# Performance work log

Measured on AMD Instinct MI355X. Metric: run time of the kernel, lower is better.

Reference implementation:

```python
import jax, jax.numpy as jnp
import numpy as np

N, E, G = 40000, 640000, 64
DIN, DH, H, DE = 64, 64, 2, 16
HD = H * DH  # 128
NEG_SLOPE_GAT = 0.2
NEG_SLOPE_ACT = 0.01
EPS_BN = 1e-5


def _p(k, shape, fan_in):
    return jax.random.normal(k, shape, dtype=jnp.float32) * (1.0 / np.sqrt(fan_in))


def setup_inputs() -> dict:
    key = jax.random.key(0)
    ks = jax.random.split(key, 32)
    inp = {
        'x': jax.random.normal(ks[0], (N, DIN), dtype=jnp.float32),
        'edge_index': jax.random.randint(ks[1], (2, E), 0, N, dtype=jnp.int32),
        'edge_attr': jax.random.normal(ks[2], (E, DE), dtype=jnp.float32),
        'batch': jnp.sort(jax.random.randint(ks[3], (N,), 0, G, dtype=jnp.int32)),
    }
    dims_in = [DIN, HD, HD]
    k = 4
    for i in (1, 2, 3):
        din = dims_in[i - 1]
        inp[f'w{i}l'] = _p(ks[k], (din, HD), din); k += 1
        inp[f'w{i}r'] = _p(ks[k], (din, HD), din); k += 1
        inp[f'w{i}e'] = _p(ks[k], (DE, HD), DE); k += 1
        inp[f'a{i}'] = _p(ks[k], (H, DH), DH); k += 1
        inp[f'cb{i}'] = jnp.zeros((HD,), dtype=jnp.float32)
        inp[f'g{i}'] = jnp.ones((HD,), dtype=jnp.float32)
        inp[f'bb{i}'] = jnp.zeros((HD,), dtype=jnp.float32)
    inp['fc1w'] = _p(ks[k], (HD, DH), HD); k += 1
    inp['fc1b'] = jnp.zeros((DH,), dtype=jnp.float32)
    inp['fc2w'] = _p(ks[k], (DH, 1), DH); k += 1
    inp['fc2b'] = jnp.zeros((1,), dtype=jnp.float32)
    return inp


def _gatv2(x, src, dst, ea, wl, wr, we, att, bias):
    # x:[N,din], src/dst:[Ef] (self-loops included), ea:[Ef,DE]
    xl = (x @ wl).reshape(-1, H, DH)            # source transform [N,H,C]
    xr = (x @ wr).reshape(-1, H, DH)            # target transform
    ee = (ea @ we).reshape(-1, H, DH)           # edge transform [Ef,H,C]
    m = xl[src] + xr[dst] + ee                  # GATv2 pre-activation [Ef,H,C]
    s = jnp.einsum('ehc,hc->eh', jax.nn.leaky_relu(m, NEG_SLOPE_GAT), att)
    smax = jax.ops.segment_max(s, dst, num_segments=N)
    ex = jnp.exp(s - smax[dst])
    den = jax.ops.segment_sum(ex, dst, num_segments=N)
    alpha = ex / (den[dst] + 1e-16)             # segment softmax over in-edges
    out = jax.ops.segment_sum(alpha[:, :, None] * xl[src], dst, num_segments=N)
    return out.reshape(-1, HD) + bias


def _bn(x, g, b):
    mu = jnp.mean(x, axis=0)
    var = jnp.mean((x - mu) ** 2, axis=0)
    return (x - mu) * jax.lax.rsqrt(var + EPS_BN) * g + b


def reference(x, edge_index, edge_attr, batch,
              w1l, w1r, w1e, a1, cb1, g1, bb1,
              w2l, w2r, w2e, a2, cb2, g2, bb2,
              w3l, w3r, w3e, a3, cb3, g3, bb3,
              fc1w, fc1b, fc2w, fc2b):
    src, dst = edge_index[0], edge_index[1]
    # add self-loops with fill_value='mean' edge attrs (mean over incoming edges)
    deg = jax.ops.segment_sum(jnp.ones((E,), jnp.float32), dst, num_segments=N)
    loop_attr = jax.ops.segment_sum(edge_attr, dst, num_segments=N) / jnp.clip(deg, 1.0)[:, None]
    ar = jnp.arange(N, dtype=src.dtype)
    src_f = jnp.concatenate([src, ar])
    dst_f = jnp.concatenate([dst, ar])
    ea_f = jnp.concatenate([edge_attr, loop_attr], axis=0)

    h = jax.nn.leaky_relu(_bn(_gatv2(x, src_f, dst_f, ea_f, w1l, w1r, w1e, a1, cb1), g1, bb1), NEG_SLOPE_ACT)
    h = jax.nn.leaky_relu(_bn(_gatv2(h, src_f, dst_f, ea_f, w2l, w2r, w2e, a2, cb2), g2, bb2), NEG_SLOPE_ACT)
    h = jax.nn.leaky_relu(_bn(_gatv2(h, src_f, dst_f, ea_f, w3l, w3r, w3e, a3, cb3), g3, bb3), NEG_SLOPE_ACT)

    # global mean pool over graphs
    cnt = jax.ops.segment_sum(jnp.ones((N,), jnp.float32), batch, num_segments=G)
    pooled = jax.ops.segment_sum(h, batch, num_segments=G) / jnp.clip(cnt, 1.0)[:, None]

    hh = jax.nn.relu(pooled @ fc1w + fc1b)  # dropout is identity at inference
    return hh @ fc2w + fc2b
```

## Files before the change

### kernel.cpp

```cpp
#include <hip/hip_runtime.h>
#include <math.h>

#define NN 40000
#define NE 640000
#define NG 64
#define DINV 64
#define HDV 128
#define DEV 16
#define EF (NE + NN)
#define PSPLIT 16

typedef float v2f __attribute__((ext_vector_type(2)));

__device__ __forceinline__ int chan_of_pos(int p) { return (p >> 1) + 64 * (p & 1); }

template <int CTRL>
__device__ __forceinline__ float dpp_mov_f(float x) {
    return __builtin_bit_cast(float,
        __builtin_amdgcn_update_dpp(0, __builtin_bit_cast(int, x), CTRL, 0xf, 0xf, true));
}
__device__ __forceinline__ float wave_sum64(float x) {
    x += dpp_mov_f<0x111>(x);
    x += dpp_mov_f<0x112>(x);
    x += dpp_mov_f<0x114>(x);
    x += dpp_mov_f<0x118>(x);
    x += dpp_mov_f<0x142>(x);
    x += dpp_mov_f<0x143>(x);
    return __builtin_bit_cast(float, __builtin_amdgcn_readlane(__builtin_bit_cast(int, x), 63));
}


__global__ void k_count(const int* __restrict__ dst, int* __restrict__ cnt) {
    int e = blockIdx.x * 256 + threadIdx.x;
    if (e < NE) atomicAdd(&cnt[dst[e]], 1);
}

__global__ __launch_bounds__(1024) void k_scan(const int* __restrict__ cnt, int* __restrict__ rowptr) {
    const int C = 40;
    int t = threadIdx.x;
    int start = t * C;
    int end = min(start + C, NN);
    int local = 0;
    for (int i = start; i < end; ++i) local += cnt[i] + 1;
    __shared__ int ssum[1024];
    ssum[t] = local;
    __syncthreads();
    for (int off = 1; off < 1024; off <<= 1) {
        int v = (t >= off) ? ssum[t - off] : 0;
        __syncthreads();
        ssum[t] += v;
        __syncthreads();
    }
    int running = (t == 0) ? 0 : ssum[t - 1];
    for (int i = start; i < end; ++i) {
        rowptr[i] = running;
        running += cnt[i] + 1;
    }
    if (end == NN && start < NN) rowptr[NN] = running;
}

__global__ void k_csr_init(const int* __restrict__ rowptr, int* __restrict__ cursor) {
    int n = blockIdx.x * 256 + threadIdx.x;
    if (n < NN) cursor[n] = rowptr[n];
}

__global__ void k_fill(const int* __restrict__ src, const int* __restrict__ dst,
                       const float* __restrict__ edge_attr,
                       int* __restrict__ cursor, int* __restrict__ csr_src, float* __restrict__ csr_ea) {
    int e = blockIdx.x * 256 + threadIdx.x;
    if (e < NE) {
        int d = dst[e];
        int p = atomicAdd(&cursor[d], 1);
        csr_src[p] = src[e];
        const float4* s4 = (const float4*)&edge_attr[(size_t)e * DEV];
        float4* d4 = (float4*)&csr_ea[(size_t)p * DEV];
        d4[0] = s4[0]; d4[1] = s4[1]; d4[2] = s4[2]; d4[3] = s4[3];
    }
}

__global__ void k_wperm_all(const float* __restrict__ w1l, const float* __restrict__ w1r,
                            const float* __restrict__ w2l, const float* __restrict__ w2r,
                            const float* __restrict__ w3l, const float* __restrict__ w3r,
                            float* __restrict__ wlp, float* __restrict__ wrp) {
    int i = blockIdx.x * 256 + threadIdx.x;
    if (i >= 3 * HDV * HDV) return;
    int layer = i / (HDV * HDV);
    int r = i - layer * HDV * HDV;
    int p = r & 127, kp = r >> 7;
    int K = (layer == 0) ? DINV : HDV;
    if (kp >= K) return;
    int kr = (layer == 0) ? kp : chan_of_pos(kp);
    int cc = chan_of_pos(p);
    const float* wl = (layer == 0) ? w1l : (layer == 1) ? w2l : w3l;
    const float* wr = (layer == 0) ? w1r : (layer == 1) ? w2r : w3r;
    wlp[i] = wl[kr * HDV + cc];
    wrp[i] = wr[kr * HDV + cc];
}

__global__ __launch_bounds__(256) void k_gemm(const float* __restrict__ A, int K,
                                              const float* __restrict__ Wl, const float* __restrict__ Wr,
                                              float* __restrict__ XL, float* __restrict__ XR,
                                              const double* __restrict__ bnsum, const double* __restrict__ bnsumsq,
                                              const float* __restrict__ g, const float* __restrict__ bb) {
    __shared__ float As[2][8][128];
    __shared__ float Bs[2][8][128];
    __shared__ float ssc[HDV], ssh[HDV];
    int t = threadIdx.x;
    if (bnsum && t < HDV) {
        int c = chan_of_pos(t);
        double mu = bnsum[t] * (1.0 / NN);
        double var = bnsumsq[t] * (1.0 / NN) - mu * mu;
        double inv = rsqrt(var + 1e-5);
        float sc = (float)(inv * (double)g[c]);
        ssc[t] = sc;
        ssh[t] = bb[c] - (float)mu * sc;
    }
    __syncthreads();
    int rb = blockIdx.x * 128;
    const float* __restrict__ Bg = blockIdx.y ? Wr : Wl;
    float* __restrict__ Xout = blockIdx.y ? XR : XL;
    int tx = t & 15, ty = t >> 4;
    int lr_ = t >> 1, lk = (t & 1) * 4;
    int bk = t >> 5, bc = (t & 31) * 4;

    auto loadA = [&](int k0) -> float4 {
        float4 av = (rb + lr_ < NN) ? *(const float4*)&A[(size_t)(rb + lr_) * K + k0 + lk]
                                    : float4{0.f, 0.f, 0.f, 0.f};
        if (bnsum) {
            int c0 = k0 + lk;
            av.x = fmaf(av.x, ssc[c0 + 0], ssh[c0 + 0]); av.x = fmaxf(av.x, 0.01f * av.x);
            av.y = fmaf(av.y, ssc[c0 + 1], ssh[c0 + 1]); av.y = fmaxf(av.y, 0.01f * av.y);
            av.z = fmaf(av.z, ssc[c0 + 2], ssh[c0 + 2]); av.z = fmaxf(av.z, 0.01f * av.z);
            av.w = fmaf(av.w, ssc[c0 + 3], ssh[c0 + 3]); av.w = fmaxf(av.w, 0.01f * av.w);
        }
        return av;
    };

    float4 av = loadA(0);
    float4 bv = *(const float4*)&Bg[(size_t)bk * HDV + bc];
    As[0][lk + 0][lr_] = av.x; As[0][lk + 1][lr_] = av.y; As[0][lk + 2][lr_] = av.z; As[0][lk + 3][lr_] = av.w;
    *(float4*)&Bs[0][bk][bc] = bv;
    __syncthreads();

    float acc[8][8] = {};
    int cur = 0;
    for (int k0 = 0; k0 < K; k0 += 8) {
        bool more = (k0 + 8) < K;
        if (more) {
            av = loadA(k0 + 8);
            bv = *(const float4*)&Bg[(size_t)(k0 + 8 + bk) * HDV + bc];
        }
        #pragma unroll
        for (int kk = 0; kk < 8; ++kk) {
            float a8[8], b8[8];
            *(float4*)&a8[0] = *(const float4*)&As[cur][kk][ty * 8];
            *(float4*)&a8[4] = *(const float4*)&As[cur][kk][ty * 8 + 4];
            *(float4*)&b8[0] = *(const float4*)&Bs[cur][kk][tx * 8];
            *(float4*)&b8[4] = *(const float4*)&Bs[cur][kk][tx * 8 + 4];
            #pragma unroll
            for (int ii = 0; ii < 8; ++ii)
                #pragma unroll
                for (int jj = 0; jj < 8; ++jj)
                    acc[ii][jj] = fmaf(a8[ii], b8[jj], acc[ii][jj]);
        }
        if (more) {
            int nxt = cur ^ 1;
            As[nxt][lk + 0][lr_] = av.x; As[nxt][lk + 1][lr_] = av.y;
            As[nxt][lk + 2][lr_] = av.z; As[nxt][lk + 3][lr_] = av.w;
            *(float4*)&Bs[nxt][bk][bc] = bv;
            __syncthreads();
            cur = nxt;
        }
    }
    #pragma unroll
    for (int ii = 0; ii < 8; ++ii) {
        int row = rb + ty * 8 + ii;
        if (row < NN) {
            float4 v0 = {acc[ii][0], acc[ii][1], acc[ii][2], acc[ii][3]};
            float4 v1 = {acc[ii][4], acc[ii][5], acc[ii][6], acc[ii][7]};
            *(float4*)&Xout[(size_t)row * HDV + tx * 8] = v0;
            *(float4*)&Xout[(size_t)row * HDV + tx * 8 + 4] = v1;
        }
    }
}

__global__ __launch_bounds__(256) void k_gat(const float* __restrict__ XL, const float* __restrict__ XR,
                                             const int* __restrict__ rowptr, const int* __restrict__ csr_src,
                                             const float* __restrict__ csr_ea,
                                             const float* __restrict__ we, const float* __restrict__ att,
                                             const float* __restrict__ cb, float* __restrict__ hpre) {
    int t = threadIdx.x;
    int L = t & 63;
    int d = __builtin_amdgcn_readfirstlane(blockIdx.x * 4 + (t >> 6));
    v2f rwe0[DEV / 2], rwe1[DEV / 2];
    #pragma unroll
    for (int j = 0; j < DEV / 2; ++j) {
        rwe0[j] = v2f{we[(2 * j) * HDV + L],      we[(2 * j + 1) * HDV + L]};
        rwe1[j] = v2f{we[(2 * j) * HDV + 64 + L], we[(2 * j + 1) * HDV + 64 + L]};
    }
    const float LOG2E = 1.4426950408889634f;
    float attv0 = att[L] * LOG2E, attv1 = att[64 + L] * LOG2E;
    v2f xr = *(const v2f*)&XR[(size_t)d * HDV + 2 * L];
    int istart = rowptr[d];
    int iend = rowptr[d + 1] - 1;
    int deg = iend - istart;
    v2f D0 = {0.f, 0.f}, D1 = {0.f, 0.f}, D2 = {0.f, 0.f}, D3 = {0.f, 0.f};
    v2f A0 = {0.f, 0.f}, A1 = {0.f, 0.f}, A2 = {0.f, 0.f}, A3 = {0.f, 0.f};
    v2f eesum = {0.f, 0.f};

    auto body = [&](int i, v2f& Dk, v2f& Ak) {
        int sx = csr_src[i];
        const v2f* eap = (const v2f*)(csr_ea + (size_t)i * DEV);
        unsigned off = ((unsigned)sx << 9) + ((unsigned)L << 3);
        v2f xl = *(const v2f*)((const char*)XL + off);
        v2f e0 = {0.f, 0.f}, e1 = {0.f, 0.f};
        #pragma unroll
        for (int j = 0; j < DEV / 2; ++j) {
            v2f ea2 = eap[j];
            e0 = __builtin_elementwise_fma(ea2, rwe0[j], e0);
            e1 = __builtin_elementwise_fma(ea2, rwe1[j], e1);
        }
        v2f eev = {e0.x + e0.y, e1.x + e1.y};
        eesum += eev;
        v2f m = xl + xr + eev;
        v2f lr = __builtin_elementwise_max(m, m * 0.2f);
        float c0 = wave_sum64(lr.x * attv0);
        float c1 = wave_sum64(lr.y * attv1);
        v2f e = {__builtin_amdgcn_exp2f(c0), __builtin_amdgcn_exp2f(c1)};
        Dk += e;
        Ak = __builtin_elementwise_fma(e, xl, Ak);
    };

    int i = istart;
    int rem = deg & 3;
    if (rem > 0) { body(i, D0, A0); ++i; }
    if (rem > 1) { body(i, D1, A1); ++i; }
    if (rem > 2) { body(i, D2, A2); ++i; }
    for (; i < iend; i += 4) {
        body(i,     D0, A0);
        body(i + 1, D1, A1);
        body(i + 2, D2, A2);
        body(i + 3, D3, A3);
    }
    {
        v2f xls = *(const v2f*)&XL[(size_t)d * HDV + 2 * L];
        v2f eeself = eesum * (1.0f / (float)max(deg, 1));
        v2f m = xls + xr + eeself;
        v2f lr = __builtin_elementwise_max(m, m * 0.2f);
        float c0 = wave_sum64(lr.x * attv0);
        float c1 = wave_sum64(lr.y * attv1);
        v2f e = {__builtin_amdgcn_exp2f(c0), __builtin_amdgcn_exp2f(c1)};
        D0 += e;
        A0 = __builtin_elementwise_fma(e, xls, A0);
    }
    v2f D = (D0 + D1) + (D2 + D3);
    v2f A = (A0 + A1) + (A2 + A3);
    v2f h = A / (D + 1e-16f) + v2f{cb[L], cb[64 + L]};
    *(v2f*)&hpre[(size_t)d * HDV + 2 * L] = h;
}


__global__ __launch_bounds__(256) void k_bn_stats(const float* __restrict__ hpre,
                                                  double* __restrict__ bnsum, double* __restrict__ bnsumsq) {
    int c2 = (threadIdx.x & 63) * 2;
    int rg = threadIdx.x >> 6;
    int r0 = blockIdx.x * 250;
    v2f s = {0.f, 0.f}, q = {0.f, 0.f};
    for (int r = r0 + rg; r < r0 + 250; r += 4) {
        v2f v = *(const v2f*)&hpre[(size_t)r * HDV + c2];
        s += v;
        q = __builtin_elementwise_fma(v, v, q);
    }
    __shared__ v2f ls[256], lq[256];
    ls[threadIdx.x] = s; lq[threadIdx.x] = q;
    __syncthreads();
    if (rg == 0) {
        int b = threadIdx.x;
        s = ls[b] + ls[b + 64] + ls[b + 128] + ls[b + 192];
        q = lq[b] + lq[b + 64] + lq[b + 128] + lq[b + 192];
        atomicAdd(&bnsum[c2],     (double)s.x);
        atomicAdd(&bnsum[c2 + 1], (double)s.y);
        atomicAdd(&bnsumsq[c2],     (double)q.x);
        atomicAdd(&bnsumsq[c2 + 1], (double)q.y);
    }
}


__global__ void k_gbounds(const int* __restrict__ batch, int* __restrict__ gstart) {
    int g = threadIdx.x;
    if (g > NG) return;
    int lo = 0, hi = NN;
    while (lo < hi) {
        int mid = (lo + hi) >> 1;
        if (batch[mid] < g) lo = mid + 1; else hi = mid;
    }
    gstart[g] = lo;
}

__global__ __launch_bounds__(256) void k_pool2(const float* __restrict__ hpre, const int* __restrict__ gstart,
                                               const double* __restrict__ bnsum, const double* __restrict__ bnsumsq,
                                               const float* __restrict__ g, const float* __restrict__ bb,
                                               float* __restrict__ pooled_sum) {
    __shared__ float ssc[HDV], ssh[HDV];
    int t = threadIdx.x;
    if (t < HDV) {
        int cc = chan_of_pos(t);
        double mu = bnsum[t] * (1.0 / NN);
        double var = bnsumsq[t] * (1.0 / NN) - mu * mu;
        double inv = rsqrt(var + 1e-5);
        float sc = (float)(inv * (double)g[cc]);
        ssc[t] = sc;
        ssh[t] = bb[cc] - (float)mu * sc;
    }
    __syncthreads();
    int gr = blockIdx.x, slice = blockIdx.y;
    int s = gstart[gr], e = gstart[gr + 1];
    int c = t & 127, half = t >> 7;
    float sc = ssc[c], sh = ssh[c];
    float acc = 0.f;
    for (int r = s + slice * 2 + half; r < e; r += PSPLIT * 2) {
        float v = fmaf(hpre[(size_t)r * HDV + c], sc, sh);
        acc += fmaxf(v, 0.01f * v);
    }
    __shared__ float ls[256];
    ls[t] = acc;
    __syncthreads();
    if (half == 0) atomicAdd(&pooled_sum[gr * HDV + c], acc + ls[t + 128]);
}

__global__ __launch_bounds__(512) void k_mlp(const float* __restrict__ pooled_sum, const int* __restrict__ gstart,
                                             const float* __restrict__ fc1w, const float* __restrict__ fc1b,
                                             const float* __restrict__ fc2w, const float* __restrict__ fc2b,
                                             float* __restrict__ out) {
    __shared__ float pl[NG * HDV];
    __shared__ float hh[NG * 64];
    int t = threadIdx.x;
    for (int i = t; i < NG * HDV; i += 512) {
        int gr = i >> 7;
        float cnt = (float)max(gstart[gr + 1] - gstart[gr], 1);
        pl[i] = pooled_sum[i] / cnt;
    }
    __syncthreads();
    for (int i = t; i < NG * 64; i += 512) {
        int gr = i >> 6, c = i & 63;
        float s = fc1b[c];
        for (int p = 0; p < HDV; ++p)
            s += pl[gr * HDV + p] * fc1w[chan_of_pos(p) * 64 + c];
        hh[i] = s > 0.f ? s : 0.f;
    }
    __syncthreads();
    if (t < NG) {
        float s = fc2b[0];
        for (int k = 0; k < 64; ++k) s += hh[t * 64 + k] * fc2w[k];
        out[t] = s;
    }
}


extern "C" void kernel_launch(void* const* d_in, const int* in_sizes, int n_in,
                              void* d_out, int out_size, void* d_ws, size_t ws_size,
                              hipStream_t stream) {
    const float* x = (const float*)d_in[0];
    const int* ei = (const int*)d_in[1];
    const int* src = ei;
    const int* dst = ei + NE;
    const float* ea = (const float*)d_in[2];
    const int* batch = (const int*)d_in[3];
    const float* fc1w = (const float*)d_in[25];
    const float* fc1b = (const float*)d_in[26];
    const float* fc2w = (const float*)d_in[27];
    const float* fc2b = (const float*)d_in[28];
    float* out = (float*)d_out;

    char* ws = (char*)d_ws;
    size_t off = 0;
    auto alloc = [&](size_t bytes) -> void* {
        void* p = ws + off;
        off = (off + bytes + 255) & ~(size_t)255;
        return p;
    };

    int* cnt = (int*)alloc(NN * 4);
    double* bnsum = (double*)alloc(3 * HDV * 8);
    double* bnsumsq = (double*)alloc(3 * HDV * 8);
    float* pooled_sum = (float*)alloc(NG * HDV * 4);
    size_t zero_bytes = off;

    int* rowptr = (int*)alloc((NN + 1) * 4);
    int* cursor = (int*)alloc(NN * 4);
    int* gstart = (int*)alloc((NG + 1) * 4);
    float* wlp = (float*)alloc(3 * HDV * HDV * 4);
    float* wrp = (float*)alloc(3 * HDV * HDV * 4);
    int* csr_src = (int*)alloc(((size_t)EF + 16) * 4);
    float* csr_ea = (float*)alloc(((size_t)EF * DEV + 64) * 4);
    float* XLb = (float*)alloc((size_t)NN * HDV * 4);
    float* XRb = (float*)alloc((size_t)NN * HDV * 4);
    float* hpre = (float*)alloc((size_t)NN * HDV * 4);
    (void)ws_size; (void)in_sizes; (void)n_in; (void)out_size;

    hipMemsetAsync(d_ws, 0, zero_bytes, stream);

    k_count<<<(NE + 255) / 256, 256, 0, stream>>>(dst, cnt);
    k_scan<<<1, 1024, 0, stream>>>(cnt, rowptr);
    k_csr_init<<<(NN + 255) / 256, 256, 0, stream>>>(rowptr, cursor);
    k_fill<<<(NE + 255) / 256, 256, 0, stream>>>(src, dst, ea, cursor, csr_src, csr_ea);
    k_gbounds<<<1, 128, 0, stream>>>(batch, gstart);
    k_wperm_all<<<(3 * HDV * HDV + 255) / 256, 256, 0, stream>>>(
        (const float*)d_in[4], (const float*)d_in[5],
        (const float*)d_in[11], (const float*)d_in[12],
        (const float*)d_in[18], (const float*)d_in[19], wlp, wrp);

    const float* actp = x;
    int K = DINV;
    for (int L = 0; L < 3; ++L) {
        const float* we = (const float*)d_in[4 + 7 * L + 2];
        const float* a  = (const float*)d_in[4 + 7 * L + 3];
        const float* cb = (const float*)d_in[4 + 7 * L + 4];

        const double* bs  = (L == 0) ? nullptr : bnsum + (size_t)(L - 1) * HDV;
        const double* bsq = (L == 0) ? nullptr : bnsumsq + (size_t)(L - 1) * HDV;
        const float* gg   = (L == 0) ? nullptr : (const float*)d_in[4 + 7 * (L - 1) + 5];
        const float* bbp  = (L == 0) ? nullptr : (const float*)d_in[4 + 7 * (L - 1) + 6];

        k_gemm<<<dim3((NN + 127) / 128, 2), 256, 0, stream>>>(
            actp, K, wlp + (size_t)L * HDV * HDV, wrp + (size_t)L * HDV * HDV,
            XLb, XRb, bs, bsq, gg, bbp);
        k_gat<<<NN / 4, 256, 0, stream>>>(XLb, XRb, rowptr, csr_src, csr_ea, we, a, cb, hpre);
        k_bn_stats<<<160, 256, 0, stream>>>(hpre, bnsum + (size_t)L * HDV, bnsumsq + (size_t)L * HDV);
        actp = hpre;
        K = HDV;
    }

    k_pool2<<<dim3(NG, PSPLIT), 256, 0, stream>>>(
        hpre, gstart, bnsum + 2 * HDV, bnsumsq + 2 * HDV,
        (const float*)d_in[4 + 7 * 2 + 5], (const float*)d_in[4 + 7 * 2 + 6], pooled_sum);
    k_mlp<<<1, 512, 0, stream>>>(pooled_sum, gstart, fc1w, fc1b, fc2w, fc2b, out);
}
```

Before: 616.0 us.

## Store XL in fp16 for gathers and fold small setup kernels together

The source-side transform XL is now written by the GEMM in half precision and converted back to float in the GAT kernel, which halves the bytes of the random per-edge gathers. The GAT edge loop is unrolled by two accumulators instead of four. The cursor initialisation is merged into the scan kernel, and the graph-boundary search is merged into the weight-permutation kernel, removing two launches. Half precision adds rounding error to the aggregated features, and the smaller unroll may expose less memory parallelism.

```diff
diff --git a/kernel.cpp b/kernel.cpp
--- a/kernel.cpp
+++ b/kernel.cpp
@@ -1,4 +1,5 @@
 #include <hip/hip_runtime.h>
+#include <hip/hip_fp16.h>
 #include <math.h>
 
 #define NN 40000
@@ -35,7 +36,8 @@
     if (e < NE) atomicAdd(&cnt[dst[e]], 1);
 }
 
-__global__ __launch_bounds__(1024) void k_scan(const int* __restrict__ cnt, int* __restrict__ rowptr) {
+__global__ __launch_bounds__(1024) void k_scan(const int* __restrict__ cnt, int* __restrict__ rowptr,
+                                               int* __restrict__ cursor) {
     const int C = 40;
     int t = threadIdx.x;
     int start = t * C;
@@ -54,14 +56,10 @@
     int running = (t == 0) ? 0 : ssum[t - 1];
     for (int i = start; i < end; ++i) {
         rowptr[i] = running;
+        cursor[i] = running;
         running += cnt[i] + 1;
     }
     if (end == NN && start < NN) rowptr[NN] = running;
-}
-
-__global__ void k_csr_init(const int* __restrict__ rowptr, int* __restrict__ cursor) {
-    int n = blockIdx.x * 256 + threadIdx.x;
-    if (n < NN) cursor[n] = rowptr[n];
 }
 
 __global__ void k_fill(const int* __restrict__ src, const int* __restrict__ dst,
@@ -81,8 +79,21 @@
 __global__ void k_wperm_all(const float* __restrict__ w1l, const float* __restrict__ w1r,
                             const float* __restrict__ w2l, const float* __restrict__ w2r,
                             const float* __restrict__ w3l, const float* __restrict__ w3r,
-                            float* __restrict__ wlp, float* __restrict__ wrp) {
-    int i = blockIdx.x * 256 + threadIdx.x;
+                            float* __restrict__ wlp, float* __restrict__ wrp,
+                            const int* __restrict__ batch, int* __restrict__ gstart) {
+    int t = threadIdx.x;
+    if (blockIdx.x == gridDim.x - 1) {
+        int g = t;
+        if (g > NG) return;
+        int lo = 0, hi = NN;
+        while (lo < hi) {
+            int mid = (lo + hi) >> 1;
+            if (batch[mid] < g) lo = mid + 1; else hi = mid;
+        }
+        gstart[g] = lo;
+        return;
+    }
+    int i = blockIdx.x * 256 + t;
     if (i >= 3 * HDV * HDV) return;
     int layer = i / (HDV * HDV);
     int r = i - layer * HDV * HDV;
@@ -99,7 +110,7 @@
 
 __global__ __launch_bounds__(256) void k_gemm(const float* __restrict__ A, int K,
                                               const float* __restrict__ Wl, const float* __restrict__ Wr,
-                                              float* __restrict__ XL, float* __restrict__ XR,
+                                              __half* __restrict__ XLh, float* __restrict__ XR,
                                               const double* __restrict__ bnsum, const double* __restrict__ bnsumsq,
                                               const float* __restrict__ g, const float* __restrict__ bb) {
     __shared__ float As[2][8][128];
@@ -118,7 +129,6 @@
     __syncthreads();
     int rb = blockIdx.x * 128;
     const float* __restrict__ Bg = blockIdx.y ? Wr : Wl;
-    float* __restrict__ Xout = blockIdx.y ? XR : XL;
     int tx = t & 15, ty = t >> 4;
     int lr_ = t >> 1, lk = (t & 1) * 4;
     int bk = t >> 5, bc = (t & 31) * 4;
@@ -172,19 +182,36 @@
             cur = nxt;
         }
     }
-    #pragma unroll
-    for (int ii = 0; ii < 8; ++ii) {
-        int row = rb + ty * 8 + ii;
-        if (row < NN) {
-            float4 v0 = {acc[ii][0], acc[ii][1], acc[ii][2], acc[ii][3]};
-            float4 v1 = {acc[ii][4], acc[ii][5], acc[ii][6], acc[ii][7]};
-            *(float4*)&Xout[(size_t)row * HDV + tx * 8] = v0;
-            *(float4*)&Xout[(size_t)row * HDV + tx * 8 + 4] = v1;
-        }
-    }
-}
-
-__global__ __launch_bounds__(256) void k_gat(const float* __restrict__ XL, const float* __restrict__ XR,
+    if (blockIdx.y == 0) {
+        #pragma unroll
+        for (int ii = 0; ii < 8; ++ii) {
+            int row = rb + ty * 8 + ii;
+            if (row < NN) {
+                __half2 h4[4];
+                #pragma unroll
+                for (int jj = 0; jj < 4; ++jj)
+                    h4[jj] = __half2{__float2half_rn(acc[ii][2 * jj]), __float2half_rn(acc[ii][2 * jj + 1])};
+                *(__half2*)&XLh[(size_t)row * HDV + tx * 8 + 0] = h4[0];
+                *(__half2*)&XLh[(size_t)row * HDV + tx * 8 + 2] = h4[1];
+                *(__half2*)&XLh[(size_t)row * HDV + tx * 8 + 4] = h4[2];
+                *(__half2*)&XLh[(size_t)row * HDV + tx * 8 + 6] = h4[3];
+            }
+        }
+    } else {
+        #pragma unroll
+        for (int ii = 0; ii < 8; ++ii) {
+            int row = rb + ty * 8 + ii;
+            if (row < NN) {
+                float4 v0 = {acc[ii][0], acc[ii][1], acc[ii][2], acc[ii][3]};
+                float4 v1 = {acc[ii][4], acc[ii][5], acc[ii][6], acc[ii][7]};
+                *(float4*)&XR[(size_t)row * HDV + tx * 8] = v0;
+                *(float4*)&XR[(size_t)row * HDV + tx * 8 + 4] = v1;
+            }
+        }
+    }
+}
+
+__global__ __launch_bounds__(256) void k_gat(const __half* __restrict__ XLh, const float* __restrict__ XR,
                                              const int* __restrict__ rowptr, const int* __restrict__ csr_src,
                                              const float* __restrict__ csr_ea,
                                              const float* __restrict__ we, const float* __restrict__ att,
@@ -204,15 +231,15 @@
     int istart = rowptr[d];
     int iend = rowptr[d + 1] - 1;
     int deg = iend - istart;
-    v2f D0 = {0.f, 0.f}, D1 = {0.f, 0.f}, D2 = {0.f, 0.f}, D3 = {0.f, 0.f};
-    v2f A0 = {0.f, 0.f}, A1 = {0.f, 0.f}, A2 = {0.f, 0.f}, A3 = {0.f, 0.f};
+    v2f Da = {0.f, 0.f}, Db = {0.f, 0.f}, Aa = {0.f, 0.f}, Ab = {0.f, 0.f};
     v2f eesum = {0.f, 0.f};
 
     auto body = [&](int i, v2f& Dk, v2f& Ak) {
         int sx = csr_src[i];
         const v2f* eap = (const v2f*)(csr_ea + (size_t)i * DEV);
-        unsigned off = ((unsigned)sx << 9) + ((unsigned)L << 3);
-        v2f xl = *(const v2f*)((const char*)XL + off);
+        unsigned off = ((unsigned)sx << 8) + ((unsigned)L << 2);
+        __half2 xlh = *(const __half2*)((const char*)XLh + off);
+        v2f xl = {__half2float(xlh.x), __half2float(xlh.y)};
         v2f e0 = {0.f, 0.f}, e1 = {0.f, 0.f};
         #pragma unroll
         for (int j = 0; j < DEV / 2; ++j) {
@@ -232,29 +259,25 @@
     };
 
     int i = istart;
-    int rem = deg & 3;
-    if (rem > 0) { body(i, D0, A0); ++i; }
-    if (rem > 1) { body(i, D1, A1); ++i; }
-    if (rem > 2) { body(i, D2, A2); ++i; }
-    for (; i < iend; i += 4) {
-        body(i,     D0, A0);
-        body(i + 1, D1, A1);
-        body(i + 2, D2, A2);
-        body(i + 3, D3, A3);
+    if (deg & 1) { body(i, Da, Aa); ++i; }
+    for (; i < iend; i += 2) {
+        body(i,     Da, Aa);
+        body(i + 1, Db, Ab);
     }
     {
-        v2f xls = *(const v2f*)&XL[(size_t)d * HDV + 2 * L];
+        __half2 xlh = *(const __half2*)&XLh[(size_t)d * HDV + 2 * L];
+        v2f xls = {__half2float(xlh.x), __half2float(xlh.y)};
         v2f eeself = eesum * (1.0f / (float)max(deg, 1));
         v2f m = xls + xr + eeself;
         v2f lr = __builtin_elementwise_max(m, m * 0.2f);
         float c0 = wave_sum64(lr.x * attv0);
         float c1 = wave_sum64(lr.y * attv1);
         v2f e = {__builtin_amdgcn_exp2f(c0), __builtin_amdgcn_exp2f(c1)};
-        D0 += e;
-        A0 = __builtin_elementwise_fma(e, xls, A0);
-    }
-    v2f D = (D0 + D1) + (D2 + D3);
-    v2f A = (A0 + A1) + (A2 + A3);
+        Da += e;
+        Aa = __builtin_elementwise_fma(e, xls, Aa);
+    }
+    v2f D = Da + Db;
+    v2f A = Aa + Ab;
     v2f h = A / (D + 1e-16f) + v2f{cb[L], cb[64 + L]};
     *(v2f*)&hpre[(size_t)d * HDV + 2 * L] = h;
 }
@@ -285,17 +308,6 @@
     }
 }
 
-
-__global__ void k_gbounds(const int* __restrict__ batch, int* __restrict__ gstart) {
-    int g = threadIdx.x;
-    if (g > NG) return;
-    int lo = 0, hi = NN;
-    while (lo < hi) {
-        int mid = (lo + hi) >> 1;
-        if (batch[mid] < g) lo = mid + 1; else hi = mid;
-    }
-    gstart[g] = lo;
-}
 
 __global__ __launch_bounds__(256) void k_pool2(const float* __restrict__ hpre, const int* __restrict__ gstart,
                                                const double* __restrict__ bnsum, const double* __restrict__ bnsumsq,
@@ -393,7 +405,7 @@
     float* wrp = (float*)alloc(3 * HDV * HDV * 4);
     int* csr_src = (int*)alloc(((size_t)EF + 16) * 4);
     float* csr_ea = (float*)alloc(((size_t)EF * DEV + 64) * 4);
-    float* XLb = (float*)alloc((size_t)NN * HDV * 4);
+    __half* XLh = (__half*)alloc((size_t)NN * HDV * 2);
     float* XRb = (float*)alloc((size_t)NN * HDV * 4);
     float* hpre = (float*)alloc((size_t)NN * HDV * 4);
     (void)ws_size; (void)in_sizes; (void)n_in; (void)out_size;
@@ -401,14 +413,12 @@
     hipMemsetAsync(d_ws, 0, zero_bytes, stream);
 
     k_count<<<(NE + 255) / 256, 256, 0, stream>>>(dst, cnt);
-    k_scan<<<1, 1024, 0, stream>>>(cnt, rowptr);
-    k_csr_init<<<(NN + 255) / 256, 256, 0, stream>>>(rowptr, cursor);
+    k_scan<<<1, 1024, 0, stream>>>(cnt, rowptr, cursor);
     k_fill<<<(NE + 255) / 256, 256, 0, stream>>>(src, dst, ea, cursor, csr_src, csr_ea);
-    k_gbounds<<<1, 128, 0, stream>>>(batch, gstart);
-    k_wperm_all<<<(3 * HDV * HDV + 255) / 256, 256, 0, stream>>>(
+    k_wperm_all<<<(3 * HDV * HDV + 255) / 256 + 1, 256, 0, stream>>>(
         (const float*)d_in[4], (const float*)d_in[5],
         (const float*)d_in[11], (const float*)d_in[12],
-        (const float*)d_in[18], (const float*)d_in[19], wlp, wrp);
+        (const float*)d_in[18], (const float*)d_in[19], wlp, wrp, batch, gstart);
 
     const float* actp = x;
     int K = DINV;
@@ -424,8 +434,8 @@
 
         k_gemm<<<dim3((NN + 127) / 128, 2), 256, 0, stream>>>(
             actp, K, wlp + (size_t)L * HDV * HDV, wrp + (size_t)L * HDV * HDV,
-            XLb, XRb, bs, bsq, gg, bbp);
-        k_gat<<<NN / 4, 256, 0, stream>>>(XLb, XRb, rowptr, csr_src, csr_ea, we, a, cb, hpre);
+            XLh, XRb, bs, bsq, gg, bbp);
+        k_gat<<<NN / 4, 256, 0, stream>>>(XLh, XRb, rowptr, csr_src, csr_ea, we, a, cb, hpre);
         k_bn_stats<<<160, 256, 0, stream>>>(hpre, bnsum + (size_t)L * HDV, bnsumsq + (size_t)L * HDV);
         actp = hpre;
         K = HDV;
```

Result: faster. 602.3 us (-2.2%).
